# Performance work log

Hardware: AMD Instinct MI355X
Metric: run time of the kernel (lower is better)

The kernel has to match this reference:

```python
import jax, jax.numpy as jnp
import numpy as np

K = 20          # args.k (minu=True)
EPS = 1e-5      # BatchNorm eps
BNS = float(1.0 / np.sqrt(1.0 + EPS))  # eval-mode BN with running_mean=0, running_var=1


def knn_idx(x, k):
    # x: (B, C, N); returns indices of k nearest neighbors (incl. self): (B, N, k)
    xx = jnp.sum(x * x, axis=1)                       # (B, N)
    inner = jnp.einsum('bcn,bcm->bnm', x, x)          # (B, N, N)
    dist = 2.0 * inner - xx[:, :, None] - xx[:, None, :]  # = -||xi - xj||^2
    return jax.lax.top_k(dist, k)[1]


def graph_feature(x, k):
    # x: (B, C, N) -> edge features (B, 2C, N, k) = cat(neighbor - center, center)
    idx = knn_idx(x, k)                               # (B, N, k)
    xt = jnp.transpose(x, (0, 2, 1))                  # (B, N, C)
    feat = jnp.take_along_axis(xt[:, None, :, :], idx[..., None], axis=2)  # (B, N, k, C)
    center = xt[:, :, None, :]
    out = jnp.concatenate([feat - center, jnp.broadcast_to(center, feat.shape)], axis=-1)
    return jnp.transpose(out, (0, 3, 1, 2))


def edge_block(x, w, g, b, k):
    # EdgeConv: gather -> 1x1 conv -> BN(eval) -> LeakyReLU(0.2) -> max over neighbors
    h = graph_feature(x, k)                           # (B, 2C, N, k)
    y = jnp.einsum('bcnk,oc->bonk', h, w)
    y = g[None, :, None, None] * (y * BNS) + b[None, :, None, None]
    y = jax.nn.leaky_relu(y, 0.2)
    return jnp.max(y, axis=-1)                        # (B, O, N)


def _bn1(v, g, b):
    return g * (v * BNS) + b


def setup_inputs() -> dict:
    key = jax.random.key(0)
    ks = jax.random.split(key, 32)
    B, C, N = 16, 6, 1024

    def w(k_, shape):
        return jax.random.normal(k_, shape, jnp.float32) / np.sqrt(shape[1])

    def gm(k_, n):
        return 1.0 + 0.1 * jax.random.normal(k_, (n,), jnp.float32)

    def bt(k_, n):
        return 0.1 * jax.random.normal(k_, (n,), jnp.float32)

    return {
        'x': jax.random.normal(ks[0], (B, C, N), jnp.float32),
        'disc': jax.random.normal(ks[1], (B, 1), jnp.float32),
        'w1': w(ks[2], (64, 12)),   'g1': gm(ks[3], 64),   'b1': bt(ks[4], 64),
        'w2': w(ks[5], (64, 128)),  'g2': gm(ks[6], 64),   'b2': bt(ks[7], 64),
        'w3': w(ks[8], (128, 128)), 'g3': gm(ks[9], 128),  'b3': bt(ks[10], 128),
        'w4': w(ks[11], (256, 256)),'g4': gm(ks[12], 256), 'b4': bt(ks[13], 256),
        'w5': w(ks[14], (1024, 512)),'g5': gm(ks[15], 1024),'b5': bt(ks[16], 1024),
        'wl1': w(ks[17], (256, 2048)),'g6': gm(ks[18], 256),'b6': bt(ks[19], 256),
        'wl2': w(ks[20], (128, 256)),'g7': gm(ks[21], 128),'b7': bt(ks[22], 128),
        'wl21': w(ks[23], (64, 128)),
        'wl22': w(ks[24], (32, 64)),'g8': gm(ks[25], 32), 'b8': bt(ks[26], 32),
        'wl3': w(ks[27], (90, 32)),
    }


def reference(x, disc, w1, g1, b1, w2, g2, b2, w3, g3, b3, w4, g4, b4,
              w5, g5, b5, wl1, g6, b6, wl2, g7, b7, wl21, wl22, g8, b8, wl3):
    # disc is accepted by the original forward but unused
    x1 = edge_block(x, w1, g1, b1, K)                 # (B, 64, N)
    x2 = edge_block(x1, w2, g2, b2, K)                # (B, 64, N)
    x3 = edge_block(x2, w3, g3, b3, K)                # (B, 128, N)
    x4 = edge_block(x3, w4, g4, b4, K)                # (B, 256, N)
    h = jnp.concatenate([x1, x2, x3, x4], axis=1)     # (B, 512, N)
    y = jnp.einsum('bcn,oc->bon', h, w5)              # conv5 1x1
    y = g5[None, :, None] * (y * BNS) + b5[None, :, None]
    y = jax.nn.leaky_relu(y, 0.2)                     # (B, emb, N)
    p = jnp.concatenate([jnp.max(y, axis=2), jnp.mean(y, axis=2)], axis=1)  # (B, 2*emb)
    z = jax.nn.leaky_relu(_bn1(p @ wl1.T, g6, b6), 0.2)
    z = jax.nn.leaky_relu(_bn1(z @ wl2.T, g7, b7), 0.2)
    z = jax.nn.gelu(_bn1((z @ wl21.T) @ wl22.T, g8, b8), approximate=False)
    return z @ wl3.T                                  # (B, 90)
```

## Files before the change

### kernel.cpp

```cpp
#include <hip/hip_runtime.h>
#include <math.h>
#include <float.h>

#define BNS_C 0.9999950000374996f

typedef __bf16 bf8 __attribute__((ext_vector_type(8)));
typedef float f4 __attribute__((ext_vector_type(4)));
union I4BF8 { int4 i; bf8 b; };

static __device__ __forceinline__ unsigned short f2bf(float f) {
    unsigned u = __float_as_uint(f);
    u += 0x7fff + ((u >> 16) & 1);
    return (unsigned short)(u >> 16);
}

__global__ void k_xin_t(const float* __restrict__ x, float* __restrict__ X0, float* __restrict__ xx) {
    int i = blockIdx.x * 256 + threadIdx.x;
    int b = i >> 10, n = i & 1023;
    const float* xb = x + (((size_t)b * 6) << 10) + n;
    float4* o4 = (float4*)(X0 + ((size_t)i << 3));
    float v0 = xb[0], v1 = xb[1 << 10], v2 = xb[2 << 10];
    float v3 = xb[3 << 10], v4 = xb[4 << 10], v5 = xb[5 << 10];
    o4[0] = make_float4(v0, v1, v2, v3);
    o4[1] = make_float4(v4, v5, 0.f, 0.f);
    xx[i] = v0*v0 + v1*v1 + v2*v2 + v3*v3 + v4*v4 + v5*v5;
}

__global__ __launch_bounds__(256) void k_gram2(const float* __restrict__ X, const float* __restrict__ xx,
                                               float* __restrict__ D, int Cp, int b0) {
    int z = blockIdx.z, b = b0 + z;
    int n0 = blockIdx.y * 64, m0 = blockIdx.x * 64;
    __shared__ float As[64][33], Bs[64][33];
    int tid = threadIdx.x;
    int ti = tid & 15, tj = tid >> 4;
    float acc[4][4] = {};
    const float* Xb = X + (((size_t)b) << 10) * Cp;
    for (int c0 = 0; c0 < Cp; c0 += 32) {
        for (int e = tid; e < 2048; e += 256) {
            int row = e >> 5, cc = e & 31, c = c0 + cc;
            float a = 0.f, bb = 0.f;
            if (c < Cp) {
                a  = Xb[(size_t)(n0 + row) * Cp + c];
                bb = Xb[(size_t)(m0 + row) * Cp + c];
            }
            As[row][cc] = a; Bs[row][cc] = bb;
        }
        __syncthreads();
#pragma unroll 8
        for (int cc = 0; cc < 32; ++cc) {
            float xv[4], yv[4];
#pragma unroll
            for (int a = 0; a < 4; ++a) xv[a] = As[tj + 16 * a][cc];
#pragma unroll
            for (int q = 0; q < 4; ++q) yv[q] = Bs[ti + 16 * q][cc];
#pragma unroll
            for (int a = 0; a < 4; ++a)
#pragma unroll
                for (int q = 0; q < 4; ++q) acc[a][q] += xv[a] * yv[q];
        }
        __syncthreads();
    }
#pragma unroll
    for (int a = 0; a < 4; ++a) {
        int n = n0 + tj + 16 * a;
        float xn = xx[(b << 10) + n];
#pragma unroll
        for (int q = 0; q < 4; ++q) {
            int m = m0 + ti + 16 * q;
            D[((size_t)((z << 10) + n) << 10) + m] = 2.f * acc[a][q] - xn - xx[(b << 10) + m];
        }
    }
}

__global__ __launch_bounds__(256) void k_topk(const float* __restrict__ D, int* __restrict__ idxo, int b0) {
    const int K = 20;
    int lane = threadIdx.x & 63;
    int rl = blockIdx.x * 4 + (threadIdx.x >> 6);
    const float* row = D + ((size_t)rl << 10);
    float d[16];
#pragma unroll
    for (int j = 0; j < 16; ++j) d[j] = row[lane + 64 * j];
    int rg = (b0 << 10) + rl;
    for (int it = 0; it < K; ++it) {
        float bv = d[0]; int bj = 0;
#pragma unroll
        for (int j = 1; j < 16; ++j) if (d[j] > bv) { bv = d[j]; bj = j; }
        int bm = lane + (bj << 6);
        for (int off = 32; off > 0; off >>= 1) {
            float ov = __shfl_down(bv, off);
            int   om = __shfl_down(bm, off);
            if (ov > bv || (ov == bv && om < bm)) { bv = ov; bm = om; }
        }
        bm = __shfl(bm, 0);
        if (lane == 0) idxo[rg * K + it] = bm;
        if ((bm & 63) == lane) d[bm >> 6] = -FLT_MAX;
    }
}

__global__ __launch_bounds__(256) void k_uv(const float* __restrict__ X, const float* __restrict__ w,
                                            float* __restrict__ V, float* __restrict__ U,
                                            int Cp, int C, int O) {
    int n0 = blockIdx.x * 64, o0 = blockIdx.y * 64, b = blockIdx.z;
    __shared__ float Xs[64][33], Was[64][33], Wds[64][33];
    int tid = threadIdx.x, ti = tid & 15, tj = tid >> 4;
    float accv[4][4] = {}, accu[4][4] = {};
    const float* Xb = X + (((size_t)b) << 10) * Cp;
    int W2 = 2 * C;
    for (int c0 = 0; c0 < Cp; c0 += 32) {
        for (int e = tid; e < 2048; e += 256) {
            int row = e >> 5, cc = e & 31, c = c0 + cc;
            Xs[row][cc] = (c < Cp) ? Xb[(size_t)(n0 + row) * Cp + c] : 0.f;
            float wa = 0.f, wd = 0.f;
            if (c < C) {
                float a_ = w[(size_t)(o0 + row) * W2 + c];
                float b_ = w[(size_t)(o0 + row) * W2 + C + c];
                wa = a_; wd = b_ - a_;
            }
            Was[row][cc] = wa; Wds[row][cc] = wd;
        }
        __syncthreads();
#pragma unroll 8
        for (int cc = 0; cc < 32; ++cc) {
            float xv[4], av[4], dv[4];
#pragma unroll
            for (int a = 0; a < 4; ++a) xv[a] = Xs[tj + 16 * a][cc];
#pragma unroll
            for (int q = 0; q < 4; ++q) { av[q] = Was[ti + 16 * q][cc]; dv[q] = Wds[ti + 16 * q][cc]; }
#pragma unroll
            for (int a = 0; a < 4; ++a)
#pragma unroll
                for (int q = 0; q < 4; ++q) { accv[a][q] += xv[a] * av[q]; accu[a][q] += xv[a] * dv[q]; }
        }
        __syncthreads();
    }
#pragma unroll
    for (int a = 0; a < 4; ++a) {
        int n = n0 + tj + 16 * a;
#pragma unroll
        for (int q = 0; q < 4; ++q) {
            int o = o0 + ti + 16 * q;
            size_t oi = ((size_t)((b << 10) + n)) * O + o;
            V[oi] = accv[a][q]; U[oi] = accu[a][q];
        }
    }
}

__global__ __launch_bounds__(256) void k_gmax(const float* __restrict__ V, const float* __restrict__ U,
                                              const int* __restrict__ idx,
                                              const float* __restrict__ gg, const float* __restrict__ bb,
                                              float* __restrict__ Xo, float* __restrict__ xx,
                                              unsigned short* __restrict__ HB, int coff, int O) {
    __shared__ float sxx[4];
    int tid = threadIdx.x;
    int Tn = 256 / O;
    int j = tid / O, o = tid - j * O;
    int pt = blockIdx.x * Tn + j;
    int b = pt >> 10;
    float uv = U[(size_t)pt * O + o];
    float gv = gg[o], bv = bb[o];
    const int* ip = idx + (size_t)pt * 20;
    float mx = -FLT_MAX;
    for (int k = 0; k < 20; ++k) {
        int m = ip[k] & 1023;
        float vv = V[(size_t)((b << 10) + m) * O + o];
        float y = gv * ((vv + uv) * BNS_C) + bv;
        y = y > 0.f ? y : 0.2f * y;
        mx = fmaxf(mx, y);
    }
    Xo[(size_t)pt * O + o] = mx;
    HB[(size_t)pt * 512 + coff + o] = f2bf(mx);
    float s = mx * mx;
#pragma unroll
    for (int off = 32; off; off >>= 1) s += __shfl_down(s, off);
    int wid = tid >> 6, lane = tid & 63;
    if (lane == 0) sxx[wid] = s;
    __syncthreads();
    if (o == 0) {
        int Wpp = O >> 6;
        float t = 0.f;
        for (int w = 0; w < Wpp; ++w) t += sxx[j * Wpp + w];
        xx[pt] = t;
    }
}

__global__ __launch_bounds__(256) void k_final_mfma(const unsigned short* __restrict__ HB,
                                                    const float* __restrict__ w5,
                                                    const float* __restrict__ g5,
                                                    const float* __restrict__ b5,
                                                    float* __restrict__ pp) {
    int b = blockIdx.x;
    int nt = blockIdx.z;
    int wv = threadIdx.x >> 6, lane = threadIdx.x & 63;
    int r = lane & 15, q = lane >> 4;
    int o = blockIdx.y * 64 + wv * 16 + r;
    bf8 Bfr[16];
    const float* wrow = w5 + (size_t)o * 512 + q * 8;
#pragma unroll
    for (int s = 0; s < 16; ++s) {
        float4 f0 = *(const float4*)(wrow + s * 32);
        float4 f1 = *(const float4*)(wrow + s * 32 + 4);
        I4BF8 u_;
        u_.i.x = f2bf(f0.x) | ((unsigned)f2bf(f0.y) << 16);
        u_.i.y = f2bf(f0.z) | ((unsigned)f2bf(f0.w) << 16);
        u_.i.z = f2bf(f1.x) | ((unsigned)f2bf(f1.y) << 16);
        u_.i.w = f2bf(f1.z) | ((unsigned)f2bf(f1.w) << 16);
        Bfr[s] = u_.b;
    }
    float gb = g5[o] * BNS_C, bv = b5[o];
    const unsigned short* HBb = HB + ((((size_t)b) << 10) + (nt << 8)) * 512 + q * 8;
    float mx = -FLT_MAX, sm = 0.f;
    for (int g = 0; g < 4; ++g) {
        const unsigned short* a0 = HBb + (size_t)(g * 64 +  0 + r) * 512;
        const unsigned short* a1 = HBb + (size_t)(g * 64 + 16 + r) * 512;
        const unsigned short* a2 = HBb + (size_t)(g * 64 + 32 + r) * 512;
        const unsigned short* a3 = HBb + (size_t)(g * 64 + 48 + r) * 512;
        f4 C0 = {0.f, 0.f, 0.f, 0.f}, C1 = C0, C2 = C0, C3 = C0;
#pragma unroll
        for (int s = 0; s < 16; ++s) {
            I4BF8 A0, A1, A2, A3;
            A0.i = *(const int4*)(a0 + s * 32);
            A1.i = *(const int4*)(a1 + s * 32);
            A2.i = *(const int4*)(a2 + s * 32);
            A3.i = *(const int4*)(a3 + s * 32);
            C0 = __builtin_amdgcn_mfma_f32_16x16x32_bf16(A0.b, Bfr[s], C0, 0, 0, 0);
            C1 = __builtin_amdgcn_mfma_f32_16x16x32_bf16(A1.b, Bfr[s], C1, 0, 0, 0);
            C2 = __builtin_amdgcn_mfma_f32_16x16x32_bf16(A2.b, Bfr[s], C2, 0, 0, 0);
            C3 = __builtin_amdgcn_mfma_f32_16x16x32_bf16(A3.b, Bfr[s], C3, 0, 0, 0);
        }
#pragma unroll
        for (int e = 0; e < 4; ++e) {
            float y0 = gb * C0[e] + bv; y0 = y0 > 0.f ? y0 : 0.2f * y0; mx = fmaxf(mx, y0); sm += y0;
            float y1 = gb * C1[e] + bv; y1 = y1 > 0.f ? y1 : 0.2f * y1; mx = fmaxf(mx, y1); sm += y1;
            float y2 = gb * C2[e] + bv; y2 = y2 > 0.f ? y2 : 0.2f * y2; mx = fmaxf(mx, y2); sm += y2;
            float y3 = gb * C3[e] + bv; y3 = y3 > 0.f ? y3 : 0.2f * y3; mx = fmaxf(mx, y3); sm += y3;
        }
    }
    mx = fmaxf(mx, __shfl_down(mx, 32)); sm += __shfl_down(sm, 32);
    mx = fmaxf(mx, __shfl_down(mx, 16)); sm += __shfl_down(sm, 16);
    if (q == 0) {
        float* pb = pp + (size_t)(nt * 16 + b) * 2048;
        pb[o] = mx;
        pb[1024 + o] = sm;
    }
}

__global__ void k_pfinal(const float* __restrict__ pp, float* __restrict__ p) {
    int i = blockIdx.x * 256 + threadIdx.x;
    int b = i >> 10, o = i & 1023;
    float mx = -FLT_MAX, sm = 0.f;
    for (int nt = 0; nt < 4; ++nt) {
        const float* q = pp + (size_t)(nt * 16 + b) * 2048;
        mx = fmaxf(mx, q[o]); sm += q[1024 + o];
    }
    p[b * 2048 + o] = mx;
    p[b * 2048 + 1024 + o] = sm * (1.f / 1024.f);
}

__global__ __launch_bounds__(256) void k_fc2(const float* __restrict__ in, const float* __restrict__ w,
                                             const float* __restrict__ gg, const float* __restrict__ bb,
                                             float* __restrict__ out,
                                             int R, int C, int O, int act) {
    int gw = blockIdx.x * 4 + (threadIdx.x >> 6);
    int lane = threadIdx.x & 63;
    if (gw >= R * O) return;
    int r = gw / O, o = gw - r * O;
    const float* ir = in + (size_t)r * C;
    const float* wr = w + (size_t)o * C;
    float s = 0.f;
    for (int c = lane; c < C; c += 64) s += ir[c] * wr[c];
#pragma unroll
    for (int off = 32; off; off >>= 1) s += __shfl_down(s, off);
    if (lane == 0) {
        float y = s;
        if (gg) y = gg[o] * (s * BNS_C) + bb[o];
        if (act == 1) y = y > 0.f ? y : 0.2f * y;
        else if (act == 2) y = 0.5f * y * (1.f + erff(y * 0.70710678118654752f));
        out[gw] = y;
    }
}

__global__ __launch_bounds__(256) void k_fc_tail(const float* __restrict__ z1,
                                                 const float* __restrict__ wl2, const float* __restrict__ g7, const float* __restrict__ b7,
                                                 const float* __restrict__ wl21,
                                                 const float* __restrict__ wl22, const float* __restrict__ g8, const float* __restrict__ b8,
                                                 const float* __restrict__ wl3,
                                                 float* __restrict__ out) {
    __shared__ float L0[4096];
    __shared__ float L1[2048];
    __shared__ float L2[1024];
    __shared__ float L3[512];
    int tid = threadIdx.x;
    for (int i = tid; i < 4096; i += 256) L0[i] = z1[i];
    __syncthreads();
    for (int idx = tid; idx < 2048; idx += 256) {
        int o = idx >> 4, r = idx & 15;
        const float* wr = wl2 + (size_t)o * 256;
        const float* ir = L0 + r * 256;
        float s = 0.f;
        for (int c = 0; c < 256; ++c) s += ir[c] * wr[c];
        float y = g7[o] * (s * BNS_C) + b7[o];
        L1[r * 128 + o] = y > 0.f ? y : 0.2f * y;
    }
    __syncthreads();
    for (int idx = tid; idx < 1024; idx += 256) {
        int o = idx >> 4, r = idx & 15;
        const float* wr = wl21 + (size_t)o * 128;
        const float* ir = L1 + r * 128;
        float s = 0.f;
        for (int c = 0; c < 128; ++c) s += ir[c] * wr[c];
        L2[r * 64 + o] = s;
    }
    __syncthreads();
    for (int idx = tid; idx < 512; idx += 256) {
        int o = idx >> 4, r = idx & 15;
        const float* wr = wl22 + (size_t)o * 64;
        const float* ir = L2 + r * 64;
        float s = 0.f;
        for (int c = 0; c < 64; ++c) s += ir[c] * wr[c];
        float y = g8[o] * (s * BNS_C) + b8[o];
        L3[r * 32 + o] = 0.5f * y * (1.f + erff(y * 0.70710678118654752f));
    }
    __syncthreads();
    for (int idx = tid; idx < 1440; idx += 256) {
        int o = idx / 16, r = idx & 15;
        const float* wr = wl3 + (size_t)o * 32;
        const float* ir = L3 + r * 32;
        float s = 0.f;
        for (int c = 0; c < 32; ++c) s += ir[c] * wr[c];
        out[r * 90 + o] = s;
    }
}

extern "C" void kernel_launch(void* const* d_in, const int* in_sizes, int n_in,
                              void* d_out, int out_size, void* d_ws, size_t ws_size,
                              hipStream_t stream) {
    typedef const float* fp;
    fp x  = (fp)d_in[0];
    fp w1 = (fp)d_in[2],  g1 = (fp)d_in[3],  b1 = (fp)d_in[4];
    fp w2 = (fp)d_in[5],  g2 = (fp)d_in[6],  b2 = (fp)d_in[7];
    fp w3 = (fp)d_in[8],  g3 = (fp)d_in[9],  b3 = (fp)d_in[10];
    fp w4 = (fp)d_in[11], g4 = (fp)d_in[12], b4 = (fp)d_in[13];
    fp w5 = (fp)d_in[14], g5 = (fp)d_in[15], b5 = (fp)d_in[16];
    fp wl1 = (fp)d_in[17], g6 = (fp)d_in[18], b6 = (fp)d_in[19];
    fp wl2 = (fp)d_in[20], g7 = (fp)d_in[21], b7 = (fp)d_in[22];
    fp wl21 = (fp)d_in[23], wl22 = (fp)d_in[24];
    fp g8 = (fp)d_in[25], b8 = (fp)d_in[26], wl3 = (fp)d_in[27];

    char* ws = (char*)d_ws;
    size_t off = 0;
    auto alloc = [&](size_t floats) { float* p_ = (float*)(ws + off); off += floats * 4; off = (off + 255) & ~(size_t)255; return p_; };
    float* X0  = alloc(131072);
    float* X1  = alloc(1048576);
    float* X2  = alloc(1048576);
    float* X3  = alloc(2097152);
    float* X4  = alloc(4194304);
    float* xx  = alloc(16384);
    int*   nbr = (int*)alloc(327680);
    unsigned short* HB = (unsigned short*)alloc(4194304);
    float* pp  = alloc(131072);
    float* p   = alloc(32768);
    float* z1  = alloc(4096);
    size_t poolAvail = (ws_size > off) ? (ws_size - off) / 4 : 0;
    int fullD = poolAvail >= 16777216;
    float* pool = alloc(fullD ? 16777216 : 8388608);

    float* D = pool;
    float* V = pool;
    float* U = pool + 4194304;

    k_xin_t<<<64, 256, 0, stream>>>(x, X0, xx);

    struct Blk { const float* Xin; int Cp, C, O, coff; const float *w, *g, *b; float* Xout; };
    Blk blks[4] = {
        {X0, 8,   6,   64,  0,   w1, g1, b1, X1},
        {X1, 64,  64,  64,  64,  w2, g2, b2, X2},
        {X2, 64,  64,  128, 128, w3, g3, b3, X3},
        {X3, 128, 128, 256, 256, w4, g4, b4, X4},
    };
    for (int i = 0; i < 4; ++i) {
        const Blk& B_ = blks[i];
        if (fullD) {
            k_gram2<<<dim3(16, 16, 16), 256, 0, stream>>>(B_.Xin, xx, D, B_.Cp, 0);
            k_topk<<<4096, 256, 0, stream>>>(D, nbr, 0);
        } else {
            for (int b0 = 0; b0 < 16; b0 += 8) {
                k_gram2<<<dim3(16, 16, 8), 256, 0, stream>>>(B_.Xin, xx, D, B_.Cp, b0);
                k_topk<<<2048, 256, 0, stream>>>(D, nbr, b0);
            }
        }
        k_uv<<<dim3(16, B_.O / 64, 16), 256, 0, stream>>>(B_.Xin, B_.w, V, U, B_.Cp, B_.C, B_.O);
        int Tn = 256 / B_.O;
        k_gmax<<<16384 / Tn, 256, 0, stream>>>(V, U, nbr, B_.g, B_.b, B_.Xout, xx, HB, B_.coff, B_.O);
    }

    k_final_mfma<<<dim3(16, 16, 4), 256, 0, stream>>>(HB, w5, g5, b5, pp);
    k_pfinal<<<64, 256, 0, stream>>>(pp, p);

    k_fc2<<<(16 * 256 + 3) / 4, 256, 0, stream>>>(p, wl1, g6, b6, z1, 16, 2048, 256, 1);
    k_fc_tail<<<1, 256, 0, stream>>>(z1, wl2, g7, b7, wl21, wl22, g8, b8, wl3, (float*)d_out);
}
```

Measured before the change: 1.035 ms.

## Tile HB into 32-channel slabs, fuse pooling reduction into fc1, reorder tail loops

The concatenated bf16 feature buffer is now stored as per-batch slabs of 32 channels by 1024 points, so each MFMA A-fragment load in the final conv reads contiguous 64-byte rows instead of rows strided by 512 channels. The separate partial-pool reduction kernel is removed and folded into the first FC kernel, which combines the four partial max/sum tiles on the fly, saving a launch and an intermediate buffer. The tail FC loops are reindexed so consecutive threads walk output channels. The fused FC recomputes the pool reduction for every output neuron, adding redundant global reads.

```diff
diff --git a/kernel.cpp b/kernel.cpp
--- a/kernel.cpp
+++ b/kernel.cpp
@@ -155,7 +155,7 @@
     int Tn = 256 / O;
     int j = tid / O, o = tid - j * O;
     int pt = blockIdx.x * Tn + j;
-    int b = pt >> 10;
+    int b = pt >> 10, n = pt & 1023;
     float uv = U[(size_t)pt * O + o];
     float gv = gg[o], bv = bb[o];
     const int* ip = idx + (size_t)pt * 20;
@@ -168,7 +168,8 @@
         mx = fmaxf(mx, y);
     }
     Xo[(size_t)pt * O + o] = mx;
-    HB[(size_t)pt * 512 + coff + o] = f2bf(mx);
+    int c = coff + o;
+    HB[(((size_t)(b * 16 + (c >> 5)) << 10) + n) * 32 + (c & 31)] = f2bf(mx);
     float s = mx * mx;
 #pragma unroll
     for (int off = 32; off; off >>= 1) s += __shfl_down(s, off);
@@ -207,21 +208,18 @@
         Bfr[s] = u_.b;
     }
     float gb = g5[o] * BNS_C, bv = b5[o];
-    const unsigned short* HBb = HB + ((((size_t)b) << 10) + (nt << 8)) * 512 + q * 8;
     float mx = -FLT_MAX, sm = 0.f;
     for (int g = 0; g < 4; ++g) {
-        const unsigned short* a0 = HBb + (size_t)(g * 64 +  0 + r) * 512;
-        const unsigned short* a1 = HBb + (size_t)(g * 64 + 16 + r) * 512;
-        const unsigned short* a2 = HBb + (size_t)(g * 64 + 32 + r) * 512;
-        const unsigned short* a3 = HBb + (size_t)(g * 64 + 48 + r) * 512;
+        int row0 = (nt << 8) + (g << 6);
         f4 C0 = {0.f, 0.f, 0.f, 0.f}, C1 = C0, C2 = C0, C3 = C0;
 #pragma unroll
         for (int s = 0; s < 16; ++s) {
+            const unsigned short* slab = HB + (((size_t)(b * 16 + s) << 10) + row0) * 32 + q * 8;
             I4BF8 A0, A1, A2, A3;
-            A0.i = *(const int4*)(a0 + s * 32);
-            A1.i = *(const int4*)(a1 + s * 32);
-            A2.i = *(const int4*)(a2 + s * 32);
-            A3.i = *(const int4*)(a3 + s * 32);
+            A0.i = *(const int4*)(slab + (size_t)( 0 + r) * 32);
+            A1.i = *(const int4*)(slab + (size_t)(16 + r) * 32);
+            A2.i = *(const int4*)(slab + (size_t)(32 + r) * 32);
+            A3.i = *(const int4*)(slab + (size_t)(48 + r) * 32);
             C0 = __builtin_amdgcn_mfma_f32_16x16x32_bf16(A0.b, Bfr[s], C0, 0, 0, 0);
             C1 = __builtin_amdgcn_mfma_f32_16x16x32_bf16(A1.b, Bfr[s], C1, 0, 0, 0);
             C2 = __builtin_amdgcn_mfma_f32_16x16x32_bf16(A2.b, Bfr[s], C2, 0, 0, 0);
@@ -244,38 +242,29 @@
     }
 }
 
-__global__ void k_pfinal(const float* __restrict__ pp, float* __restrict__ p) {
-    int i = blockIdx.x * 256 + threadIdx.x;
-    int b = i >> 10, o = i & 1023;
-    float mx = -FLT_MAX, sm = 0.f;
-    for (int nt = 0; nt < 4; ++nt) {
-        const float* q = pp + (size_t)(nt * 16 + b) * 2048;
-        mx = fmaxf(mx, q[o]); sm += q[1024 + o];
-    }
-    p[b * 2048 + o] = mx;
-    p[b * 2048 + 1024 + o] = sm * (1.f / 1024.f);
-}
-
-__global__ __launch_bounds__(256) void k_fc2(const float* __restrict__ in, const float* __restrict__ w,
-                                             const float* __restrict__ gg, const float* __restrict__ bb,
-                                             float* __restrict__ out,
-                                             int R, int C, int O, int act) {
+__global__ __launch_bounds__(256) void k_fc2p(const float* __restrict__ pp, const float* __restrict__ w,
+                                              const float* __restrict__ gg, const float* __restrict__ bb,
+                                              float* __restrict__ out, int O) {
     int gw = blockIdx.x * 4 + (threadIdx.x >> 6);
     int lane = threadIdx.x & 63;
-    if (gw >= R * O) return;
     int r = gw / O, o = gw - r * O;
-    const float* ir = in + (size_t)r * C;
-    const float* wr = w + (size_t)o * C;
+    const float* wr = w + (size_t)o * 2048;
     float s = 0.f;
-    for (int c = lane; c < C; c += 64) s += ir[c] * wr[c];
+    for (int c = lane; c < 2048; c += 64) {
+        const float* q0 = pp + (size_t)r * 2048 + c;
+        float v;
+        if (c < 1024) {
+            v = fmaxf(fmaxf(q0[0], q0[16 * 2048]), fmaxf(q0[32 * 2048], q0[48 * 2048]));
+        } else {
+            v = (q0[0] + q0[16 * 2048] + q0[32 * 2048] + q0[48 * 2048]) * (1.f / 1024.f);
+        }
+        s += v * wr[c];
+    }
 #pragma unroll
     for (int off = 32; off; off >>= 1) s += __shfl_down(s, off);
     if (lane == 0) {
-        float y = s;
-        if (gg) y = gg[o] * (s * BNS_C) + bb[o];
-        if (act == 1) y = y > 0.f ? y : 0.2f * y;
-        else if (act == 2) y = 0.5f * y * (1.f + erff(y * 0.70710678118654752f));
-        out[gw] = y;
+        float y = gg[o] * (s * BNS_C) + bb[o];
+        out[gw] = y > 0.f ? y : 0.2f * y;
     }
 }
 
@@ -293,7 +282,7 @@
     for (int i = tid; i < 4096; i += 256) L0[i] = z1[i];
     __syncthreads();
     for (int idx = tid; idx < 2048; idx += 256) {
-        int o = idx >> 4, r = idx & 15;
+        int r = idx >> 7, o = idx & 127;
         const float* wr = wl2 + (size_t)o * 256;
         const float* ir = L0 + r * 256;
         float s = 0.f;
@@ -303,7 +292,7 @@
     }
     __syncthreads();
     for (int idx = tid; idx < 1024; idx += 256) {
-        int o = idx >> 4, r = idx & 15;
+        int r = idx >> 6, o = idx & 63;
         const float* wr = wl21 + (size_t)o * 128;
         const float* ir = L1 + r * 128;
         float s = 0.f;
@@ -312,7 +301,7 @@
     }
     __syncthreads();
     for (int idx = tid; idx < 512; idx += 256) {
-        int o = idx >> 4, r = idx & 15;
+        int r = idx >> 5, o = idx & 31;
         const float* wr = wl22 + (size_t)o * 64;
         const float* ir = L2 + r * 64;
         float s = 0.f;
@@ -322,7 +311,7 @@
     }
     __syncthreads();
     for (int idx = tid; idx < 1440; idx += 256) {
-        int o = idx / 16, r = idx & 15;
+        int r = idx / 90, o = idx - r * 90;
         const float* wr = wl3 + (size_t)o * 32;
         const float* ir = L3 + r * 32;
         float s = 0.f;
@@ -358,7 +347,6 @@
     int*   nbr = (int*)alloc(327680);
     unsigned short* HB = (unsigned short*)alloc(4194304);
     float* pp  = alloc(131072);
-    float* p   = alloc(32768);
     float* z1  = alloc(4096);
     size_t poolAvail = (ws_size > off) ? (ws_size - off) / 4 : 0;
     int fullD = poolAvail >= 16777216;
@@ -394,8 +382,7 @@
     }
 
     k_final_mfma<<<dim3(16, 16, 4), 256, 0, stream>>>(HB, w5, g5, b5, pp);
-    k_pfinal<<<64, 256, 0, stream>>>(pp, p);
-
-    k_fc2<<<(16 * 256 + 3) / 4, 256, 0, stream>>>(p, wl1, g6, b6, z1, 16, 2048, 256, 1);
+
+    k_fc2p<<<(16 * 256) / 4, 256, 0, stream>>>(pp, wl1, g6, b6, z1, 256);
     k_fc_tail<<<1, 256, 0, stream>>>(z1, wl2, g7, b7, wl21, wl22, g8, b8, wl3, (float*)d_out);
 }
```

Measured after the change: 993.0 us. 4.1% less time.
